# Kernel optimization log

Hardware: AMD Instinct MI355X
Metric: run time of the kernel (lower is better)

The kernel has to match this reference:

```python
import jax, jax.numpy as jnp
import numpy as np

D_MODEL = 1024
N_HEADS = 16


def setup_inputs() -> dict:
    key = jax.random.key(0)
    ks = jax.random.split(key, 11)
    B, S, D = 2, 2048, D_MODEL
    scale = 1.0 / np.sqrt(D)
    inp = {
        "q": jax.random.normal(ks[0], (B, S, D), jnp.float32),
        "k": jax.random.normal(ks[1], (B, S, D), jnp.float32),
        "v": jax.random.normal(ks[2], (B, S, D), jnp.float32),
        "W_q": jax.random.normal(ks[3], (D, D), jnp.float32) * scale,
        "b_q": jnp.zeros((D,), jnp.float32),
        "W_k": jax.random.normal(ks[4], (D, D), jnp.float32) * scale,
        "b_k": jnp.zeros((D,), jnp.float32),
        "W_v": jax.random.normal(ks[5], (D, D), jnp.float32) * scale,
        "b_v": jnp.zeros((D,), jnp.float32),
        "W_o": jax.random.normal(ks[6], (D, D), jnp.float32) * scale,
        "b_o": jnp.zeros((D,), jnp.float32),
    }
    return inp


def reference(q, k, v, W_q, b_q, W_k, b_k, W_v, b_v, W_o, b_o):
    B, S, D = q.shape
    H = N_HEADS
    d_k = D // H
    # linear projections, then split heads: [B, H, S, d_k]
    def proj(x, W, b):
        y = jnp.einsum("bsd,de->bse", x, W.T) + b
        return y.reshape(B, S, H, d_k).transpose(0, 2, 1, 3)
    Q = proj(q, W_q, b_q)
    K = proj(k, W_k, b_k)
    V = proj(v, W_v, b_v)
    # scaled dot-product attention with explicit [B,H,S,S] scores
    scores = jnp.einsum("bhqd,bhkd->bhqk", Q, K) / jnp.sqrt(jnp.float32(d_k))
    attn = jax.nn.softmax(scores, axis=-1)
    out = jnp.einsum("bhqk,bhkd->bhqd", attn, V)
    out = out.transpose(0, 2, 1, 3).reshape(B, S, D)
    return jnp.einsum("bsd,de->bse", out, W_o.T) + b_o
```

## Files before the change

### kernel.cpp

```cpp
#include <hip/hip_runtime.h>
#include <hip/hip_bf16.h>
#include <math.h>

typedef __bf16 bf16_t;
typedef bf16_t bf16x8 __attribute__((ext_vector_type(8)));
typedef float f32x4 __attribute__((ext_vector_type(4)));

#define D_MODEL 1024
#define NH 16
#define DK 64
#define SEQ 2048
#define MROWS 4096
#define LDSW 64
#define LDC 136
#define KT 32

__device__ __forceinline__ bf16x8 ldfrag(const bf16_t* p) {
    union { uint4 u; bf16x8 v; } c;
    c.u = *reinterpret_cast<const uint4*>(p);
    return c.v;
}

__device__ __forceinline__ f32x4 zero4() { f32x4 z = {0.f, 0.f, 0.f, 0.f}; return z; }

__device__ __forceinline__ void gll16(const bf16_t* g, bf16_t* l) {
    __builtin_amdgcn_global_load_lds(
        (const __attribute__((address_space(1))) unsigned int*)g,
        (__attribute__((address_space(3))) unsigned int*)l,
        16, 0, 0);
}

__global__ void pack3(const float* __restrict__ a, const float* __restrict__ b,
                      const float* __restrict__ c,
                      bf16_t* __restrict__ da, bf16_t* __restrict__ db, bf16_t* __restrict__ dc) {
    const float* s = (blockIdx.y == 0) ? a : (blockIdx.y == 1) ? b : c;
    bf16_t* d      = (blockIdx.y == 0) ? da : (blockIdx.y == 1) ? db : dc;
    int i = (blockIdx.x * blockDim.x + threadIdx.x) * 4;
    float4 f = *reinterpret_cast<const float4*>(s + i);
    union { bf16_t h[4]; uint2 u; } o;
    o.h[0] = (bf16_t)f.x; o.h[1] = (bf16_t)f.y; o.h[2] = (bf16_t)f.z; o.h[3] = (bf16_t)f.w;
    *reinterpret_cast<uint2*>(d + i) = o.u;
}

__global__ void pack4(const float* __restrict__ a, const float* __restrict__ b,
                      const float* __restrict__ c, const float* __restrict__ e,
                      bf16_t* __restrict__ da, bf16_t* __restrict__ db,
                      bf16_t* __restrict__ dc, bf16_t* __restrict__ de) {
    const float* s = (blockIdx.y == 0) ? a : (blockIdx.y == 1) ? b : (blockIdx.y == 2) ? c : e;
    bf16_t* d      = (blockIdx.y == 0) ? da : (blockIdx.y == 1) ? db : (blockIdx.y == 2) ? dc : de;
    int i = (blockIdx.x * blockDim.x + threadIdx.x) * 4;
    float4 f = *reinterpret_cast<const float4*>(s + i);
    union { bf16_t h[4]; uint2 u; } o;
    o.h[0] = (bf16_t)f.x; o.h[1] = (bf16_t)f.y; o.h[2] = (bf16_t)f.z; o.h[3] = (bf16_t)f.w;
    *reinterpret_cast<uint2*>(d + i) = o.u;
}

__device__ __forceinline__ void gemm_core(
    const bf16_t* __restrict__ A, const bf16_t* __restrict__ Bm,
    int K, int m0, int n0,
    bf16_t* As, bf16_t* Bs,
    f32x4 acc[4][4]) {

    const int tid = threadIdx.x;
    const int lane = tid & 63;
    const int wid = tid >> 6;
    const int wm = (wid >> 1) * 64, wn = (wid & 1) * 64;
    const int l15 = lane & 15, quad = lane >> 4;

    const int lrow   = lane >> 3;
    const int gcol   = ((lane & 7) ^ lrow) * 8;

    #pragma unroll
    for (int i = 0; i < 4; i++)
        #pragma unroll
        for (int j = 0; j < 4; j++) acc[i][j] = zero4();

    #pragma unroll
    for (int t = 0; t < 4; t++) {
        const int rbase = wid * 32 + t * 8;
        gll16(A  + (size_t)(m0 + rbase + lrow) * K + gcol, As + rbase * LDSW);
        gll16(Bm + (size_t)(n0 + rbase + lrow) * K + gcol, Bs + rbase * LDSW);
    }

    int kt = 0;
    for (int k0 = 0; k0 < K; k0 += 64, kt++) {
        __syncthreads();
        const int cur = (kt & 1) * 128 * LDSW;
        if (k0 + 64 < K) {
            const int nxt = ((kt + 1) & 1) * 128 * LDSW;
            #pragma unroll
            for (int t = 0; t < 4; t++) {
                const int rbase = wid * 32 + t * 8;
                gll16(A  + (size_t)(m0 + rbase + lrow) * K + k0 + 64 + gcol, As + nxt + rbase * LDSW);
                gll16(Bm + (size_t)(n0 + rbase + lrow) * K + k0 + 64 + gcol, Bs + nxt + rbase * LDSW);
            }
        }
        #pragma unroll
        for (int c = 0; c < 2; c++) {
            bf16x8 af[4], bfr[4];
            #pragma unroll
            for (int i = 0; i < 4; i++) {
                const int row = wm + i * 16 + l15;
                const int pc = ((c * 4 + quad) ^ (l15 & 7)) * 8;
                af[i] = ldfrag(As + cur + row * LDSW + pc);
            }
            #pragma unroll
            for (int j = 0; j < 4; j++) {
                const int row = wn + j * 16 + l15;
                const int pc = ((c * 4 + quad) ^ (l15 & 7)) * 8;
                bfr[j] = ldfrag(Bs + cur + row * LDSW + pc);
            }
            #pragma unroll
            for (int i = 0; i < 4; i++)
                #pragma unroll
                for (int j = 0; j < 4; j++)
                    acc[i][j] = __builtin_amdgcn_mfma_f32_16x16x32_bf16(af[i], bfr[j], acc[i][j], 0, 0, 0);
        }
    }
}

__global__ __launch_bounds__(256, 2) void proj_gemm(
    const bf16_t* __restrict__ qb, const bf16_t* __restrict__ kb,
    const bf16_t* __restrict__ vb,
    const bf16_t* __restrict__ Wq, const bf16_t* __restrict__ Wk,
    const bf16_t* __restrict__ Wv,
    const float* __restrict__ bq, const float* __restrict__ bk, const float* __restrict__ bv,
    bf16_t* __restrict__ Qh, bf16_t* __restrict__ Kh, bf16_t* __restrict__ Vt) {

    __shared__ __align__(16) bf16_t sm[4 * 128 * LDSW];
    bf16_t* As = sm;
    bf16_t* Bs = sm + 2 * 128 * LDSW;
    bf16_t (*Cs)[LDC] = reinterpret_cast<bf16_t(*)[LDC]>(sm);
    f32x4 acc[4][4];

    const int mode = blockIdx.z;
    const bf16_t* X = (mode == 0) ? qb : (mode == 1) ? kb : vb;
    const bf16_t* W = (mode == 0) ? Wq : (mode == 1) ? Wk : Wv;
    const float* bias = (mode == 0) ? bq : (mode == 1) ? bk : bv;
    const int m0 = blockIdx.y * 128, n0 = blockIdx.x * 128;

    gemm_core(X, W, D_MODEL, m0, n0, As, Bs, acc);

    const int tid = threadIdx.x, lane = tid & 63, wid = tid >> 6;
    const int wm = (wid >> 1) * 64, wn = (wid & 1) * 64;
    const int l15 = lane & 15, quad = lane >> 4;

    __syncthreads();
    if (mode != 2) {
        const float sc = (mode == 0) ? 0.125f * 1.44269504f : 1.0f;
        #pragma unroll
        for (int i = 0; i < 4; i++)
            #pragma unroll
            for (int j = 0; j < 4; j++)
                #pragma unroll
                for (int r = 0; r < 4; r++) {
                    int gn = n0 + wn + j * 16 + l15;
                    Cs[wm + i * 16 + quad * 4 + r][wn + j * 16 + l15] =
                        (bf16_t)((acc[i][j][r] + bias[gn]) * sc);
                }
    } else {
        #pragma unroll
        for (int i = 0; i < 4; i++)
            #pragma unroll
            for (int j = 0; j < 4; j++)
                #pragma unroll
                for (int r = 0; r < 4; r++) {
                    int gn = n0 + wn + j * 16 + l15;
                    Cs[wn + j * 16 + l15][wm + i * 16 + quad * 4 + r] =
                        (bf16_t)(acc[i][j][r] + bias[gn]);
                }
    }
    __syncthreads();

    #pragma unroll
    for (int c = tid; c < 2048; c += 256) {
        int row = c >> 4, col8 = (c & 15) << 3;
        uint4 val = *reinterpret_cast<const uint4*>(&Cs[row][col8]);
        if (mode != 2) {
            int gm = m0 + row, gn = n0 + col8;
            int b = gm >> 11, seq = gm & 2047;
            int h = gn >> 6, dk = gn & 63;
            bf16_t* dst = (mode == 0) ? Qh : Kh;
            *reinterpret_cast<uint4*>(dst + ((size_t)(b * NH + h) * SEQ + seq) * DK + dk) = val;
        } else {
            int gn = n0 + row, gm = m0 + col8;
            int b = gm >> 11, seq = gm & 2047;
            int h = gn >> 6, dk = gn & 63;
            *reinterpret_cast<uint4*>(Vt + ((size_t)(b * NH + h) * DK + dk) * SEQ + seq) = val;
        }
    }
}

__global__ __launch_bounds__(256, 2) void out_gemm(
    const bf16_t* __restrict__ Oc, const bf16_t* __restrict__ Wo,
    const float* __restrict__ bo, float* __restrict__ Cout) {

    __shared__ __align__(16) bf16_t As[2 * 128 * LDSW];
    __shared__ __align__(16) bf16_t Bs[2 * 128 * LDSW];
    f32x4 acc[4][4];
    const int m0 = blockIdx.y * 128, n0 = blockIdx.x * 128;

    gemm_core(Oc, Wo, D_MODEL, m0, n0, As, Bs, acc);

    const int tid = threadIdx.x, lane = tid & 63, wid = tid >> 6;
    const int wm = (wid >> 1) * 64, wn = (wid & 1) * 64;
    const int l15 = lane & 15, quad = lane >> 4;

    #pragma unroll
    for (int i = 0; i < 4; i++)
        #pragma unroll
        for (int j = 0; j < 4; j++)
            #pragma unroll
            for (int r = 0; r < 4; r++) {
                int gm = m0 + wm + i * 16 + quad * 4 + r;
                int gn = n0 + wn + j * 16 + l15;
                Cout[(size_t)gm * D_MODEL + gn] = acc[i][j][r] + bo[gn];
            }
}

__global__ __launch_bounds__(256) void attn_kernel(
    const bf16_t* __restrict__ Qh, const bf16_t* __restrict__ Kh,
    const bf16_t* __restrict__ Vt, bf16_t* __restrict__ Oc) {

    __shared__ __align__(16) bf16_t Ks[2 * KT * 64];
    __shared__ __align__(16) bf16_t Vts[2 * 64 * KT];
    __shared__ __align__(16) bf16_t Pls[64 * KT];

    const int tid = threadIdx.x, lane = tid & 63, wid = tid >> 6;
    const int l15 = lane & 15, quad = lane >> 4;
    const int bh = blockIdx.x;
    const int q0 = blockIdx.y * 64;
    const bf16_t* Qbase = Qh + (size_t)bh * SEQ * DK;
    const bf16_t* Kbase = Kh + (size_t)bh * SEQ * DK;
    const bf16_t* Vbase = Vt + (size_t)bh * DK * SEQ;

    const int krow  = lane >> 3;
    const int kgcol = ((lane & 7) ^ krow) * 8;
    const int vrow  = lane >> 2;
    const int vgcol = ((lane & 3) ^ ((vrow >> 1) & 3)) * 8;

    bf16x8 aQ[2];
    #pragma unroll
    for (int c = 0; c < 2; c++)
        aQ[c] = ldfrag(Qbase + (size_t)(q0 + wid * 16 + l15) * DK + c * 32 + quad * 8);

    f32x4 oacc[4];
    #pragma unroll
    for (int j = 0; j < 4; j++) oacc[j] = zero4();
    float l_i[4] = {0.f, 0.f, 0.f, 0.f};

    gll16(Kbase + (size_t)(wid * 8 + krow) * DK + kgcol,  Ks  + (wid * 8) * 64);
    gll16(Vbase + (size_t)(wid * 16 + vrow) * SEQ + vgcol, Vts + (wid * 16) * KT);

    for (int kt = 0; kt < SEQ / KT; kt++) {
        __syncthreads();
        const int curK = (kt & 1) * KT * 64;
        const int curV = (kt & 1) * 64 * KT;
        if (kt + 1 < SEQ / KT) {
            const int k1 = (kt + 1) * KT;
            const int nxtK = ((kt + 1) & 1) * KT * 64;
            const int nxtV = ((kt + 1) & 1) * 64 * KT;
            gll16(Kbase + (size_t)(k1 + wid * 8 + krow) * DK + kgcol,  Ks  + nxtK + (wid * 8) * 64);
            gll16(Vbase + (size_t)(wid * 16 + vrow) * SEQ + k1 + vgcol, Vts + nxtV + (wid * 16) * KT);
        }

        f32x4 sacc[2];
        sacc[0] = zero4(); sacc[1] = zero4();
        #pragma unroll
        for (int c = 0; c < 2; c++) {
            bf16x8 bk2[2];
            #pragma unroll
            for (int j = 0; j < 2; j++) {
                const int pc = ((c * 4 + quad) ^ (l15 & 7)) * 8;
                bk2[j] = ldfrag(Ks + curK + (j * 16 + l15) * 64 + pc);
            }
            #pragma unroll
            for (int j = 0; j < 2; j++)
                sacc[j] = __builtin_amdgcn_mfma_f32_16x16x32_bf16(
                    aQ[c], bk2[j], sacc[j], 0, 0, 0);
        }

        #pragma unroll
        for (int r = 0; r < 4; r++) {
            float e0 = exp2f(sacc[0][r]);
            float e1 = exp2f(sacc[1][r]);
            l_i[r] += e0 + e1;
            const int prow = wid * 16 + quad * 4 + r;
            const int sw = (prow ^ (prow >> 2)) & 3;
            bf16_t* pbase = Pls + prow * KT;
            const int hi = l15 >> 3, lo = l15 & 7;
            pbase[((hi) ^ sw) * 8 + lo]     = (bf16_t)e0;
            pbase[((2 + hi) ^ sw) * 8 + lo] = (bf16_t)e1;
        }

        {
            const int swp = (l15 ^ (l15 >> 2)) & 3;
            bf16x8 ap = ldfrag(Pls + (wid * 16 + l15) * KT + ((quad ^ swp) * 8));
            #pragma unroll
            for (int j = 0; j < 4; j++) {
                const int pv = (quad ^ ((l15 >> 1) & 3)) * 8;
                bf16x8 bv = ldfrag(Vts + curV + (j * 16 + l15) * KT + pv);
                oacc[j] = __builtin_amdgcn_mfma_f32_16x16x32_bf16(
                    ap, bv, oacc[j], 0, 0, 0);
            }
        }
    }

    __syncthreads();
    bf16_t* Osm = Ks;
    #pragma unroll
    for (int r = 0; r < 4; r++) {
        float l = l_i[r];
        #pragma unroll
        for (int off = 1; off < 16; off <<= 1)
            l += __shfl_xor(l, off, 64);
        float inv = 1.0f / l;
        const int prow = wid * 16 + quad * 4 + r;
        const int sw = prow & 7;
        const int hi = l15 >> 3, lo = l15 & 7;
        #pragma unroll
        for (int j = 0; j < 4; j++)
            Osm[prow * 64 + (((2 * j + hi) ^ sw) * 8) + lo] = (bf16_t)(oacc[j][r] * inv);
    }
    __syncthreads();

    const int b = bh >> 4, h = bh & 15;
    #pragma unroll
    for (int c = tid; c < 512; c += 256) {
        int row = c >> 3, col8 = c & 7;
        uint4 val = *reinterpret_cast<const uint4*>(Osm + row * 64 + ((col8 ^ (row & 7)) << 3));
        *reinterpret_cast<uint4*>(Oc + ((size_t)(b * SEQ + q0 + row)) * D_MODEL + h * DK + (col8 << 3)) = val;
    }
}

extern "C" void kernel_launch(void* const* d_in, const int* in_sizes, int n_in,
                              void* d_out, int out_size, void* d_ws, size_t ws_size,
                              hipStream_t stream) {
    const float* q  = (const float*)d_in[0];
    const float* k  = (const float*)d_in[1];
    const float* v  = (const float*)d_in[2];
    const float* Wq = (const float*)d_in[3];
    const float* bq = (const float*)d_in[4];
    const float* Wk = (const float*)d_in[5];
    const float* bk = (const float*)d_in[6];
    const float* Wv = (const float*)d_in[7];
    const float* bv = (const float*)d_in[8];
    const float* Wo = (const float*)d_in[9];
    const float* bo = (const float*)d_in[10];

    const size_t nx = (size_t)MROWS * D_MODEL;
    const size_t nw = (size_t)D_MODEL * D_MODEL;

    bf16_t* qb  = (bf16_t*)d_ws;
    bf16_t* kb  = qb  + nx;
    bf16_t* vb  = kb  + nx;
    bf16_t* Wqb = vb  + nx;
    bf16_t* Wkb = Wqb + nw;
    bf16_t* Wvb = Wkb + nw;
    bf16_t* Wob = Wvb + nw;
    bf16_t* Qh  = Wob + nw;
    bf16_t* Kh  = Qh  + nx;
    bf16_t* Vt  = Kh  + nx;
    bf16_t* Oc  = Vt  + nx;

    pack3<<<dim3(4096, 3), 256, 0, stream>>>(q, k, v, qb, kb, vb);
    pack4<<<dim3(1024, 4), 256, 0, stream>>>(Wq, Wk, Wv, Wo, Wqb, Wkb, Wvb, Wob);

    proj_gemm<<<dim3(8, 32, 3), 256, 0, stream>>>(qb, kb, vb, Wqb, Wkb, Wvb, bq, bk, bv, Qh, Kh, Vt);
    attn_kernel<<<dim3(32, 32), 256, 0, stream>>>(Qh, Kh, Vt, Oc);
    out_gemm<<<dim3(8, 32), 256, 0, stream>>>(Oc, Wob, bo, (float*)d_out);
}
```

Baseline: 257.4 us.

## Split attention over two key halves and merge with a combine kernel

The attention kernel now splits the key/value sequence into two halves along a new grid z dimension. Each half writes an unnormalized-weighted partial output and its per-row softmax denominator to separate buffers. A new combine kernel then blends the two partials, weighting each by its share of the total denominator. The aim is to double the number of blocks and raise concurrency or latency hiding on the GPU, at the cost of an extra kernel launch, extra workspace, and extra global traffic for the partial outputs.

```diff
diff --git a/kernel.cpp b/kernel.cpp
--- a/kernel.cpp
+++ b/kernel.cpp
@@ -14,6 +14,7 @@
 #define LDSW 64
 #define LDC 136
 #define KT 32
+#define HALFS (SEQ / 2)
 
 __device__ __forceinline__ bf16x8 ldfrag(const bf16_t* p) {
     union { uint4 u; bf16x8 v; } c;
@@ -220,7 +221,8 @@
 
 __global__ __launch_bounds__(256) void attn_kernel(
     const bf16_t* __restrict__ Qh, const bf16_t* __restrict__ Kh,
-    const bf16_t* __restrict__ Vt, bf16_t* __restrict__ Oc) {
+    const bf16_t* __restrict__ Vt, bf16_t* __restrict__ Op0,
+    bf16_t* __restrict__ Op1, float* __restrict__ lp) {
 
     __shared__ __align__(16) bf16_t Ks[2 * KT * 64];
     __shared__ __align__(16) bf16_t Vts[2 * 64 * KT];
@@ -230,8 +232,10 @@
     const int l15 = lane & 15, quad = lane >> 4;
     const int bh = blockIdx.x;
     const int q0 = blockIdx.y * 64;
+    const int half = blockIdx.z;
+    const int kbase = half * HALFS;
     const bf16_t* Qbase = Qh + (size_t)bh * SEQ * DK;
-    const bf16_t* Kbase = Kh + (size_t)bh * SEQ * DK;
+    const bf16_t* Kbase = Kh + (size_t)bh * SEQ * DK + (size_t)kbase * DK;
     const bf16_t* Vbase = Vt + (size_t)bh * DK * SEQ;
 
     const int krow  = lane >> 3;
@@ -249,19 +253,19 @@
     for (int j = 0; j < 4; j++) oacc[j] = zero4();
     float l_i[4] = {0.f, 0.f, 0.f, 0.f};
 
-    gll16(Kbase + (size_t)(wid * 8 + krow) * DK + kgcol,  Ks  + (wid * 8) * 64);
-    gll16(Vbase + (size_t)(wid * 16 + vrow) * SEQ + vgcol, Vts + (wid * 16) * KT);
-
-    for (int kt = 0; kt < SEQ / KT; kt++) {
+    gll16(Kbase + (size_t)(wid * 8 + krow) * DK + kgcol,   Ks  + (wid * 8) * 64);
+    gll16(Vbase + (size_t)(wid * 16 + vrow) * SEQ + kbase + vgcol, Vts + (wid * 16) * KT);
+
+    for (int kt = 0; kt < HALFS / KT; kt++) {
         __syncthreads();
         const int curK = (kt & 1) * KT * 64;
         const int curV = (kt & 1) * 64 * KT;
-        if (kt + 1 < SEQ / KT) {
+        if (kt + 1 < HALFS / KT) {
             const int k1 = (kt + 1) * KT;
             const int nxtK = ((kt + 1) & 1) * KT * 64;
             const int nxtV = ((kt + 1) & 1) * 64 * KT;
             gll16(Kbase + (size_t)(k1 + wid * 8 + krow) * DK + kgcol,  Ks  + nxtK + (wid * 8) * 64);
-            gll16(Vbase + (size_t)(wid * 16 + vrow) * SEQ + k1 + vgcol, Vts + nxtV + (wid * 16) * KT);
+            gll16(Vbase + (size_t)(wid * 16 + vrow) * SEQ + kbase + k1 + vgcol, Vts + nxtV + (wid * 16) * KT);
         }
 
         f32x4 sacc[2];
@@ -308,6 +312,7 @@
 
     __syncthreads();
     bf16_t* Osm = Ks;
+    float* lrow = lp + ((size_t)half * 32 + bh) * SEQ + q0;
     #pragma unroll
     for (int r = 0; r < 4; r++) {
         float l = l_i[r];
@@ -316,6 +321,7 @@
             l += __shfl_xor(l, off, 64);
         float inv = 1.0f / l;
         const int prow = wid * 16 + quad * 4 + r;
+        if (l15 == 0) lrow[prow] = l;
         const int sw = prow & 7;
         const int hi = l15 >> 3, lo = l15 & 7;
         #pragma unroll
@@ -324,13 +330,36 @@
     }
     __syncthreads();
 
+    bf16_t* Odst = half ? Op1 : Op0;
     const int b = bh >> 4, h = bh & 15;
     #pragma unroll
     for (int c = tid; c < 512; c += 256) {
         int row = c >> 3, col8 = c & 7;
         uint4 val = *reinterpret_cast<const uint4*>(Osm + row * 64 + ((col8 ^ (row & 7)) << 3));
-        *reinterpret_cast<uint4*>(Oc + ((size_t)(b * SEQ + q0 + row)) * D_MODEL + h * DK + (col8 << 3)) = val;
-    }
+        *reinterpret_cast<uint4*>(Odst + ((size_t)(b * SEQ + q0 + row)) * D_MODEL + h * DK + (col8 << 3)) = val;
+    }
+}
+
+__global__ void attn_combine(bf16_t* __restrict__ Op0, const bf16_t* __restrict__ Op1,
+                             const float* __restrict__ lp) {
+    const size_t c = (size_t)blockIdx.x * 256 + threadIdx.x;
+    const int row = (int)(c >> 7);
+    const int ch  = (int)(c & 127);
+    const int b = row >> 11, seq = row & 2047;
+    const int h = ch >> 3;
+    const size_t li = ((size_t)(b * NH + h)) * SEQ + seq;
+    const float l0 = lp[li];
+    const float l1 = lp[(size_t)32 * SEQ + li];
+    const float inv = 1.0f / (l0 + l1);
+    const float w0 = l0 * inv, w1 = l1 * inv;
+    bf16_t* p0 = Op0 + (size_t)row * D_MODEL + ch * 8;
+    const bf16_t* p1 = Op1 + (size_t)row * D_MODEL + ch * 8;
+    bf16x8 a = ldfrag(p0), bfr = ldfrag(p1);
+    union { bf16_t h8[8]; uint4 u; } o;
+    #pragma unroll
+    for (int i = 0; i < 8; i++)
+        o.h8[i] = (bf16_t)((float)a[i] * w0 + (float)bfr[i] * w1);
+    *reinterpret_cast<uint4*>(p0) = o.u;
 }
 
 extern "C" void kernel_launch(void* const* d_in, const int* in_sizes, int n_in,
@@ -362,11 +391,14 @@
     bf16_t* Kh  = Qh  + nx;
     bf16_t* Vt  = Kh  + nx;
     bf16_t* Oc  = Vt  + nx;
+    bf16_t* Op1 = Oc  + nx;
+    float*  lp  = (float*)(Op1 + nx);
 
     pack3<<<dim3(4096, 3), 256, 0, stream>>>(q, k, v, qb, kb, vb);
     pack4<<<dim3(1024, 4), 256, 0, stream>>>(Wq, Wk, Wv, Wo, Wqb, Wkb, Wvb, Wob);
 
     proj_gemm<<<dim3(8, 32, 3), 256, 0, stream>>>(qb, kb, vb, Wqb, Wkb, Wvb, bq, bk, bv, Qh, Kh, Vt);
-    attn_kernel<<<dim3(32, 32), 256, 0, stream>>>(Qh, Kh, Vt, Oc);
+    attn_kernel<<<dim3(32, 32, 2), 256, 0, stream>>>(Qh, Kh, Vt, Oc, Op1, lp);
+    attn_combine<<<dim3((unsigned)(nx / 8 / 256)), 256, 0, stream>>>(Oc, Op1, lp);
     out_gemm<<<dim3(8, 32), 256, 0, stream>>>(Oc, Wob, bo, (float*)d_out);
 }
```

Measured after the change: 263.5 us. +2.4%, slower.
